# Optimization experiments

Hardware: AMD Instinct MI355X
Metric: run time of the kernel (lower is better)

Reference implementation:

```python
import jax, jax.numpy as jnp
import numpy as np
import math

B, N, C = 8, 4096, 768
H = 12
DH = C // H
M = 256
LN_EPS = 1e-5


def setup_inputs() -> dict:
    key = jax.random.key(0)
    ks = jax.random.split(key, 7)
    x = jax.random.normal(ks[0], (B, N, C), dtype=jnp.float32)
    # torch Linear weight [out,in]; store transposed for y = x @ W
    W_qkv = jax.random.normal(ks[1], (C, 3 * C), dtype=jnp.float32) * (1.0 / math.sqrt(C))
    W_proj = jax.random.normal(ks[2], (C, C), dtype=jnp.float32) * (1.0 / math.sqrt(C))
    b_proj = jnp.zeros((C,), dtype=jnp.float32)
    gamma = jnp.ones((C,), dtype=jnp.float32)
    beta = jnp.zeros((C,), dtype=jnp.float32)
    random_features = jax.random.normal(ks[3], (M, DH), dtype=jnp.float32) / math.sqrt(DH)
    return {"x": x, "W_qkv": W_qkv, "W_proj": W_proj, "b_proj": b_proj,
            "gamma": gamma, "beta": beta, "random_features": random_features}


def _phi(t, random_features):
    # t: [B, H, N, DH] -> [B, H, N, M]; phi(x) = exp(w·x - ||x||^2/2) / sqrt(M)
    norm_sq = 0.5 * jnp.sum(t * t, axis=-1, keepdims=True)
    proj = jnp.einsum('bhnd,md->bhnm', t, random_features)
    return jnp.exp(proj - norm_sq) * (1.0 / math.sqrt(M))


def reference(x, W_qkv, W_proj, b_proj, gamma, beta, random_features):
    b, n, c = x.shape
    qkv = (x @ W_qkv).reshape(b, n, 3, H, DH)
    qkv = jnp.transpose(qkv, (2, 0, 3, 1, 4))  # [3, B, H, N, DH]
    q, k, v = qkv[0], qkv[1], qkv[2]

    q_p = _phi(q, random_features)  # [B,H,N,M]
    k_p = _phi(k, random_features)  # [B,H,N,M]

    kv = jnp.einsum('bhnm,bhnd->bhmd', k_p, v)       # [B,H,M,DH]
    out = jnp.einsum('bhnm,bhmd->bhnd', q_p, kv)     # [B,H,N,DH]

    k_sum = jnp.sum(k_p, axis=2)                      # [B,H,M]
    normalizer = jnp.einsum('bhnm,bhm->bhn', q_p, k_sum)[..., None]
    out = out / (normalizer + 1e-6)

    x_attn = jnp.transpose(out, (0, 2, 1, 3)).reshape(b, n, c)
    x_attn = x_attn @ W_proj + b_proj
    # dropout is identity in eval / p=0

    y = x + x_attn
    mu = jnp.mean(y, axis=-1, keepdims=True)
    var = jnp.mean(jnp.square(y - mu), axis=-1, keepdims=True)
    return (y - mu) * jax.lax.rsqrt(var + LN_EPS) * gamma + beta
```

## Files before the change

kernel.cpp:

```cpp
#include <hip/hip_runtime.h>
#include <hip/hip_fp16.h>


#define LOG2E 1.44269504088896340736f

typedef _Float16 half8 __attribute__((ext_vector_type(8)));
typedef _Float16 half4_t __attribute__((ext_vector_type(4)));
typedef _Float16 half2_t __attribute__((ext_vector_type(2)));
typedef float f32x4 __attribute__((ext_vector_type(4)));

#if __has_builtin(__builtin_amdgcn_fdot2)
#define FDOT2(a, b, c) __builtin_amdgcn_fdot2((a), (b), (c), false)
#else
#define FDOT2(a, b, c) \
  ((float)(a)[0] * (float)(b)[0] + ((float)(a)[1] * (float)(b)[1] + (c)))
#endif

static __device__ __forceinline__ half2_t pk2(float a, float b) {
#if __has_builtin(__builtin_amdgcn_cvt_pkrtz)
  return __builtin_bit_cast(half2_t, __builtin_amdgcn_cvt_pkrtz(a, b));
#else
  half2_t r; r[0] = (_Float16)a; r[1] = (_Float16)b; return r;
#endif
}

__device__ __forceinline__ void glds16(const _Float16* g, _Float16* s) {
  __builtin_amdgcn_global_load_lds(
      (const __attribute__((address_space(1))) void*)g,
      (__attribute__((address_space(3))) unsigned int*)s,
      16, 0, 0);
}


__global__ __launch_bounds__(256)
void prep(const float* __restrict__ x, const float* __restrict__ Wqkv,
          const float* __restrict__ Wproj, const float* __restrict__ rfm,
          _Float16* __restrict__ x_h, _Float16* __restrict__ wqkvT,
          _Float16* __restrict__ wprojT, _Float16* __restrict__ rfh) {
  const long bid = blockIdx.x;
  if (bid < 24576) {
    long i = (bid * 256 + threadIdx.x) * 4;
    float4 v = *(const float4*)(x + i);
    half4_t h;
    h[0] = (_Float16)v.x; h[1] = (_Float16)v.y; h[2] = (_Float16)v.z; h[3] = (_Float16)v.w;
    *(half4_t*)(x_h + i) = h;
    return;
  }
  long idx = (bid - 24576) * 256 + threadIdx.x;
  if (idx < 1769472) {
    int k = (int)(idx / 2304), n = (int)(idx % 2304);
    wqkvT[(long)n * 768 + k] = (_Float16)Wqkv[idx];
  } else if ((idx -= 1769472) < 589824) {
    int k = (int)(idx / 768), n = (int)(idx % 768);
    wprojT[(long)n * 768 + k] = (_Float16)Wproj[idx];
  } else if ((idx -= 589824) < 16384) {
    rfh[idx] = (_Float16)rfm[idx];
  }
}


__global__ __launch_bounds__(256)
void gemm_qkv(const _Float16* __restrict__ W, const _Float16* __restrict__ X,
              _Float16* __restrict__ qh, _Float16* __restrict__ kh,
              _Float16* __restrict__ vT,
              float* __restrict__ nsqLq, float* __restrict__ nsqLk) {
  __shared__ __align__(16) _Float16 As[128 * 32];
  __shared__ __align__(16) _Float16 Bs[128 * 32];
  const int tid = threadIdx.x;
  const int w = tid >> 6, l = tid & 63;
  const int lr = l & 15, kg = l >> 4;
  const int m0 = blockIdx.x * 128;
  const int n0 = blockIdx.y * 128;
  const int wm = (w >> 1) * 64, wn = (w & 1) * 64;

  const _Float16* gA = W + (long)(m0 + w * 32 + (l >> 2)) * 768 + (l & 3) * 8;
  const _Float16* gB = X + (long)(n0 + w * 32 + (l >> 2)) * 768 + (l & 3) * 8;
  _Float16* sA = As + (w * 32) * 32;
  _Float16* sB = Bs + (w * 32) * 32;

  f32x4 acc[4][4];
#pragma unroll
  for (int t = 0; t < 4; ++t)
#pragma unroll
    for (int u = 0; u < 4; ++u) acc[t][u] = (f32x4){0.f, 0.f, 0.f, 0.f};

  for (int kc = 0; kc < 24; ++kc) {
    __syncthreads();
    glds16(gA, sA);
    glds16(gA + 16 * 768, sA + 16 * 32);
    glds16(gB, sB);
    glds16(gB + 16 * 768, sB + 16 * 32);
    gA += 32; gB += 32;
    __syncthreads();

    half8 af[4], bf[4];
#pragma unroll
    for (int t = 0; t < 4; ++t)
      af[t] = *(const half8*)(As + (wm + t * 16 + lr) * 32 + kg * 8);
#pragma unroll
    for (int u = 0; u < 4; ++u)
      bf[u] = *(const half8*)(Bs + (wn + u * 16 + lr) * 32 + kg * 8);
#pragma unroll
    for (int t = 0; t < 4; ++t)
#pragma unroll
      for (int u = 0; u < 4; ++u)
        acc[t][u] = __builtin_amdgcn_mfma_f32_16x16x32_f16(af[t], bf[u], acc[t][u], 0, 0, 0);
  }

  const int which = (m0 >= 1536) ? 2 : ((m0 >= 768) ? 1 : 0);
  const int base = (m0 - which * 768) + wm;
  const int h = base >> 6;

  if (which < 2) {
    _Float16* dst = (which == 0) ? qh : kh;
    float* nd = (which == 0) ? nsqLq : nsqLk;
    float ns[4] = {0.f, 0.f, 0.f, 0.f};
#pragma unroll
    for (int u = 0; u < 4; ++u) {
      const int tok = n0 + wn + u * 16 + lr;
      const int b_ = tok >> 12, n_ = tok & 4095;
      const long rowbase = ((long)(b_ * 12 + h) * 4096 + n_) * 64;
#pragma unroll
      for (int t = 0; t < 4; ++t) {
        half2_t h01 = pk2(acc[t][u][0], acc[t][u][1]);
        half2_t h23 = pk2(acc[t][u][2], acc[t][u][3]);
        half4_t p4; p4[0] = h01[0]; p4[1] = h01[1]; p4[2] = h23[0]; p4[3] = h23[1];
        *(half4_t*)(dst + rowbase + t * 16 + kg * 4) = p4;
#pragma unroll
        for (int r = 0; r < 4; ++r) { float f = (float)p4[r]; ns[u] += f * f; }
      }
    }
#pragma unroll
    for (int u = 0; u < 4; ++u) {
      float s = ns[u];
      s += __shfl_xor(s, 16);
      s += __shfl_xor(s, 32);
      if (kg == 0) {
        const int tok = n0 + wn + u * 16 + lr;
        const int b_ = tok >> 12, n_ = tok & 4095;
        nd[(long)(b_ * 12 + h) * 4096 + n_] = 0.5f * s * LOG2E + 4.0f;
      }
    }
  } else {
#pragma unroll
    for (int u = 0; u < 4; ++u) {
      const int tok = n0 + wn + u * 16 + lr;
      const int b_ = tok >> 12, n_ = tok & 4095;
      const long hb = (long)(b_ * 12 + h) * 64;
#pragma unroll
      for (int t = 0; t < 4; ++t)
#pragma unroll
        for (int r = 0; r < 4; ++r)
          vT[(hb + t * 16 + kg * 4 + r) * 4096 + n_] = (_Float16)acc[t][u][r];
    }
  }
}


__global__ __launch_bounds__(256)
void gemm_proj(const _Float16* __restrict__ A, const _Float16* __restrict__ BT,
               float* __restrict__ Co, const float* __restrict__ bias,
               const float* __restrict__ resid) {
  __shared__ __align__(16) _Float16 As[128 * 32];
  __shared__ __align__(16) _Float16 Bs[128 * 32];
  const int tid = threadIdx.x;
  const int w = tid >> 6, l = tid & 63;
  const int lr = l & 15, kg = l >> 4;
  const int m0 = blockIdx.y * 128;
  const int n0 = blockIdx.x * 128;
  const int wm = (w >> 1) * 64, wn = (w & 1) * 64;

  const _Float16* gA = A + (long)(m0 + w * 32 + (l >> 2)) * 768 + (l & 3) * 8;
  const _Float16* gB = BT + (long)(n0 + w * 32 + (l >> 2)) * 768 + (l & 3) * 8;
  _Float16* sA = As + (w * 32) * 32;
  _Float16* sB = Bs + (w * 32) * 32;

  f32x4 acc[4][4];
#pragma unroll
  for (int t = 0; t < 4; ++t)
#pragma unroll
    for (int u = 0; u < 4; ++u) acc[t][u] = (f32x4){0.f, 0.f, 0.f, 0.f};

  for (int kc = 0; kc < 24; ++kc) {
    __syncthreads();
    glds16(gA, sA);
    glds16(gA + 16 * 768, sA + 16 * 32);
    glds16(gB, sB);
    glds16(gB + 16 * 768, sB + 16 * 32);
    gA += 32; gB += 32;
    __syncthreads();

    half8 af[4], bf[4];
#pragma unroll
    for (int t = 0; t < 4; ++t)
      af[t] = *(const half8*)(As + (wm + t * 16 + lr) * 32 + kg * 8);
#pragma unroll
    for (int u = 0; u < 4; ++u)
      bf[u] = *(const half8*)(Bs + (wn + u * 16 + lr) * 32 + kg * 8);
#pragma unroll
    for (int t = 0; t < 4; ++t)
#pragma unroll
      for (int u = 0; u < 4; ++u)
        acc[t][u] = __builtin_amdgcn_mfma_f32_16x16x32_f16(af[t], bf[u], acc[t][u], 0, 0, 0);
  }

#pragma unroll
  for (int u = 0; u < 4; ++u) {
    const int col = n0 + wn + u * 16 + lr;
    const float bv = bias[col];
#pragma unroll
    for (int t = 0; t < 4; ++t) {
      const int row = m0 + wm + t * 16 + kg * 4;
#pragma unroll
      for (int r = 0; r < 4; ++r) {
        long idx = (long)(row + r) * 768 + col;
        Co[idx] = acc[t][u][r] + bv + resid[idx];
      }
    }
  }
}


__global__ __launch_bounds__(256)
void kv_fused(const _Float16* __restrict__ kh, const _Float16* __restrict__ vT,
              const _Float16* __restrict__ rfh, const float* __restrict__ nsqLk,
              _Float16* __restrict__ kvpart, float* __restrict__ kspart) {
  __shared__ __align__(16) _Float16 Ka[64 * 32], Kb[64 * 32];
  __shared__ __align__(16) _Float16 Va[64 * 32], Vb[64 * 32];
  __shared__ __align__(16) _Float16 P[256 * 72];
  const int chunk = blockIdx.x, bh = blockIdx.y;
  const int tid = threadIdx.x, w = tid >> 6, l = tid & 63;
  const int lr = l & 15, kg = l >> 4;
  const long khbase = (long)bh * 4096 * 64;
  const long vtbase = (long)bh * 64 * 4096;
  const half2_t ONES = {(_Float16)1.f, (_Float16)1.f};

  half8 rf[4][2];
#pragma unroll
  for (int u = 0; u < 4; ++u)
#pragma unroll
    for (int ks = 0; ks < 2; ++ks)
      rf[u][ks] = *(const half8*)(rfh + (w * 64 + u * 16 + lr) * 64 + ks * 32 + kg * 8);

  f32x4 kvacc[4][4];
#pragma unroll
  for (int mt = 0; mt < 4; ++mt)
#pragma unroll
    for (int dt = 0; dt < 4; ++dt) kvacc[mt][dt] = (f32x4){0.f, 0.f, 0.f, 0.f};
  float ksacc[4] = {0.f, 0.f, 0.f, 0.f};

  for (int t8 = 0; t8 < 8; ++t8) {
    const int nt = chunk * 512 + t8 * 64;
    __syncthreads();
    if (w == 0) {
#pragma unroll
      for (int j = 0; j < 4; ++j)
        glds16(kh + khbase + (long)(nt + j * 16 + (l >> 2)) * 64 + (l & 3) * 8, Ka + j * 512);
    } else if (w == 1) {
#pragma unroll
      for (int j = 0; j < 4; ++j)
        glds16(kh + khbase + (long)(nt + j * 16 + (l >> 2)) * 64 + 32 + (l & 3) * 8, Kb + j * 512);
    } else if (w == 2) {
#pragma unroll
      for (int j = 0; j < 4; ++j)
        glds16(vT + vtbase + (long)(j * 16 + (l >> 2)) * 4096 + nt + (l & 3) * 8, Va + j * 512);
    } else {
#pragma unroll
      for (int j = 0; j < 4; ++j)
        glds16(vT + vtbase + (long)(j * 16 + (l >> 2)) * 4096 + nt + 32 + (l & 3) * 8, Vb + j * 512);
    }
    __syncthreads();

    half8 af[4][2];
#pragma unroll
    for (int tt = 0; tt < 4; ++tt) {
      af[tt][0] = *(const half8*)(Ka + (tt * 16 + lr) * 32 + kg * 8);
      af[tt][1] = *(const half8*)(Kb + (tt * 16 + lr) * 32 + kg * 8);
    }
    f32x4 sacc[4][4];
#pragma unroll
    for (int tt = 0; tt < 4; ++tt)
#pragma unroll
      for (int u = 0; u < 4; ++u) sacc[tt][u] = (f32x4){0.f, 0.f, 0.f, 0.f};
#pragma unroll
    for (int ks = 0; ks < 2; ++ks)
#pragma unroll
      for (int tt = 0; tt < 4; ++tt)
#pragma unroll
        for (int u = 0; u < 4; ++u)
          sacc[tt][u] = __builtin_amdgcn_mfma_f32_16x16x32_f16(af[tt][ks], rf[u][ks],
                                                               sacc[tt][u], 0, 0, 0);
    float4 nsq4[4];
#pragma unroll
    for (int tt = 0; tt < 4; ++tt)
      nsq4[tt] = *(const float4*)(nsqLk + (long)bh * 4096 + nt + tt * 16 + kg * 4);
#pragma unroll
    for (int tt = 0; tt < 4; ++tt)
#pragma unroll
      for (int u = 0; u < 4; ++u) {
        float e0 = exp2f(sacc[tt][u][0] * LOG2E - nsq4[tt].x);
        float e1 = exp2f(sacc[tt][u][1] * LOG2E - nsq4[tt].y);
        float e2 = exp2f(sacc[tt][u][2] * LOG2E - nsq4[tt].z);
        float e3 = exp2f(sacc[tt][u][3] * LOG2E - nsq4[tt].w);
        half2_t h01 = pk2(e0, e1), h23 = pk2(e2, e3);
        half4_t p4; p4[0] = h01[0]; p4[1] = h01[1]; p4[2] = h23[0]; p4[3] = h23[1];
        *(half4_t*)(P + (w * 64 + u * 16 + lr) * 72 + tt * 16 + kg * 4) = p4;
      }
#pragma unroll
    for (int ks = 0; ks < 2; ++ks) {
      half8 pa[4], bv[4];
#pragma unroll
      for (int mt = 0; mt < 4; ++mt)
        pa[mt] = *(const half8*)(P + (w * 64 + mt * 16 + lr) * 72 + ks * 32 + kg * 8);
#pragma unroll
      for (int dt = 0; dt < 4; ++dt)
        bv[dt] = *(const half8*)((ks == 0 ? Va : Vb) + (dt * 16 + lr) * 32 + kg * 8);
#pragma unroll
      for (int mt = 0; mt < 4; ++mt)
#pragma unroll
        for (int dt = 0; dt < 4; ++dt)
          kvacc[mt][dt] = __builtin_amdgcn_mfma_f32_16x16x32_f16(pa[mt], bv[dt],
                                                                 kvacc[mt][dt], 0, 0, 0);
#pragma unroll
      for (int mt = 0; mt < 4; ++mt) {
        const half2_t* pp = (const half2_t*)&pa[mt];
#pragma unroll
        for (int p = 0; p < 4; ++p) ksacc[mt] = FDOT2(pp[p], ONES, ksacc[mt]);
      }
    }
  }

#pragma unroll
  for (int mt = 0; mt < 4; ++mt) {
    float v = ksacc[mt];
    v += __shfl_xor(v, 16);
    v += __shfl_xor(v, 32);
    if (l < 16) kspart[((bh * 8 + chunk) << 8) + w * 64 + mt * 16 + l] = v;
  }
#pragma unroll
  for (int mt = 0; mt < 4; ++mt)
#pragma unroll
    for (int dt = 0; dt < 4; ++dt)
#pragma unroll
      for (int r = 0; r < 4; ++r)
        kvpart[(((long)(bh * 8 + chunk) * 256) + w * 64 + mt * 16 + kg * 4 + r) * 64 +
               dt * 16 + lr] = (_Float16)kvacc[mt][dt][r];
}


__global__ __launch_bounds__(256)
void reduce_all(const _Float16* __restrict__ kvpart, const float* __restrict__ kspart,
                _Float16* __restrict__ kvT, _Float16* __restrict__ ksumh) {
  if (blockIdx.x < 6144) {
    long i = (long)blockIdx.x * 256 + threadIdx.x;
    const int bh = (int)(i >> 14);
    const int rem = (int)(i & 16383);
    const int m = rem >> 6, d = rem & 63;
    float s = 0.f;
#pragma unroll
    for (int c = 0; c < 8; ++c)
      s += (float)kvpart[(((long)bh * 8 + c) * 256 + m) * 64 + d];
    kvT[(long)bh * 16384 + d * 256 + m] = (_Float16)s;
  } else {
    int i = (blockIdx.x - 6144) * 256 + threadIdx.x;
    int bh = i >> 8, m = i & 255;
    float s = 0.f;
#pragma unroll
    for (int c = 0; c < 8; ++c) s += kspart[((bh * 8 + c) << 8) + m];
    ksumh[i] = (_Float16)s;
  }
}


__global__ __launch_bounds__(256)
void attn_fused(const _Float16* __restrict__ qh, const _Float16* __restrict__ rfh,
                const float* __restrict__ nsqLq, const _Float16* __restrict__ kvT,
                const _Float16* __restrict__ ksumh, _Float16* __restrict__ attn) {
  __shared__ __align__(16) _Float16 Qa[64 * 32], Qb[64 * 32];
  __shared__ __align__(16) _Float16 KV[64 * 264];
  __shared__ __align__(16) _Float16 KS[256];
  __shared__ __align__(16) _Float16 P[64 * 264];
  __shared__ __align__(16) float NS[64];
  const int chunk = blockIdx.x, bh = blockIdx.y;
  const int b = bh / 12, h = bh % 12;
  const int tid = threadIdx.x, w = tid >> 6, l = tid & 63;
  const int lr = l & 15, kg = l >> 4;

  {
    const int d = tid >> 2, mb = (tid & 3) * 64;
#pragma unroll
    for (int j = 0; j < 8; ++j)
      *(half8*)(KV + d * 264 + mb + j * 8) =
          *(const half8*)(kvT + (long)bh * 16384 + d * 256 + mb + j * 8);
    if (tid < 32) *(half8*)(KS + tid * 8) = *(const half8*)(ksumh + bh * 256 + tid * 8);
  }

  half8 rf[4][2];
#pragma unroll
  for (int mt = 0; mt < 4; ++mt)
#pragma unroll
    for (int ks = 0; ks < 2; ++ks)
      rf[mt][ks] = *(const half8*)(rfh + (w * 64 + mt * 16 + lr) * 64 + ks * 32 + kg * 8);

  for (int t8 = 0; t8 < 4; ++t8) {
    const int nt = chunk * 256 + t8 * 64;
    __syncthreads();
    if (w == 0) {
#pragma unroll
      for (int j = 0; j < 4; ++j)
        glds16(qh + ((long)bh * 4096 + nt + j * 16 + (l >> 2)) * 64 + (l & 3) * 8, Qa + j * 512);
    } else if (w == 1) {
#pragma unroll
      for (int j = 0; j < 4; ++j)
        glds16(qh + ((long)bh * 4096 + nt + j * 16 + (l >> 2)) * 64 + 32 + (l & 3) * 8, Qb + j * 512);
    }
    __syncthreads();

    half8 bq[4][2];
#pragma unroll
    for (int tt = 0; tt < 4; ++tt) {
      bq[tt][0] = *(const half8*)(Qa + (tt * 16 + lr) * 32 + kg * 8);
      bq[tt][1] = *(const half8*)(Qb + (tt * 16 + lr) * 32 + kg * 8);
    }
    f32x4 sacc[4][4];
#pragma unroll
    for (int mt = 0; mt < 4; ++mt)
#pragma unroll
      for (int tt = 0; tt < 4; ++tt) sacc[mt][tt] = (f32x4){0.f, 0.f, 0.f, 0.f};
#pragma unroll
    for (int ks = 0; ks < 2; ++ks)
#pragma unroll
      for (int mt = 0; mt < 4; ++mt)
#pragma unroll
        for (int tt = 0; tt < 4; ++tt)
          sacc[mt][tt] = __builtin_amdgcn_mfma_f32_16x16x32_f16(rf[mt][ks], bq[tt][ks],
                                                                sacc[mt][tt], 0, 0, 0);
    float nsqv[4];
#pragma unroll
    for (int tt = 0; tt < 4; ++tt)
      nsqv[tt] = nsqLq[(long)bh * 4096 + nt + tt * 16 + lr];
#pragma unroll
    for (int mt = 0; mt < 4; ++mt)
#pragma unroll
      for (int tt = 0; tt < 4; ++tt) {
        float e0 = exp2f(sacc[mt][tt][0] * LOG2E - nsqv[tt]);
        float e1 = exp2f(sacc[mt][tt][1] * LOG2E - nsqv[tt]);
        float e2 = exp2f(sacc[mt][tt][2] * LOG2E - nsqv[tt]);
        float e3 = exp2f(sacc[mt][tt][3] * LOG2E - nsqv[tt]);
        half2_t h01 = pk2(e0, e1), h23 = pk2(e2, e3);
        half4_t p4; p4[0] = h01[0]; p4[1] = h01[1]; p4[2] = h23[0]; p4[3] = h23[1];
        *(half4_t*)(P + (tt * 16 + lr) * 264 + w * 64 + mt * 16 + kg * 4) = p4;
      }
    __syncthreads();

    f32x4 oacc[4];
#pragma unroll
    for (int u = 0; u < 4; ++u) oacc[u] = (f32x4){0.f, 0.f, 0.f, 0.f};
    float nacc = 0.f;
#pragma unroll
    for (int ks = 0; ks < 8; ++ks) {
      half8 ap = *(const half8*)(P + (w * 16 + lr) * 264 + ks * 32 + kg * 8);
      half8 kv8 = *(const half8*)(KS + ks * 32 + kg * 8);
      const half2_t* a2 = (const half2_t*)&ap;
      const half2_t* k2 = (const half2_t*)&kv8;
#pragma unroll
      for (int p = 0; p < 4; ++p) nacc = FDOT2(a2[p], k2[p], nacc);
#pragma unroll
      for (int u = 0; u < 4; ++u) {
        half8 bkv = *(const half8*)(KV + (u * 16 + lr) * 264 + ks * 32 + kg * 8);
        oacc[u] = __builtin_amdgcn_mfma_f32_16x16x32_f16(ap, bkv, oacc[u], 0, 0, 0);
      }
    }
    nacc += __shfl_xor(nacc, 16);
    nacc += __shfl_xor(nacc, 32);
    if (l < 16) NS[w * 16 + l] = nacc;
    f32x4 n4 = *(const f32x4*)(NS + w * 16 + kg * 4);
    float inv[4];
#pragma unroll
    for (int r = 0; r < 4; ++r) inv[r] = 1.f / (n4[r] + 1e-6f);
#pragma unroll
    for (int u = 0; u < 4; ++u)
#pragma unroll
      for (int r = 0; r < 4; ++r)
        attn[((long)b * 4096 + nt + w * 16 + kg * 4 + r) * 768 + h * 64 + u * 16 + lr] =
            (_Float16)(oacc[u][r] * inv[r]);
  }
}


__global__ __launch_bounds__(256)
void ln_kernel(const float* __restrict__ y, const float* __restrict__ gamma,
               const float* __restrict__ beta, float* __restrict__ outp) {
  const int wv = threadIdx.x >> 6, l = threadIdx.x & 63;
  const long row = (long)blockIdx.x * 4 + wv;
  const float* yr = y + row * 768;
  float v[12];
  float s = 0.f;
#pragma unroll
  for (int j = 0; j < 12; ++j) { v[j] = yr[l + j * 64]; s += v[j]; }
#pragma unroll
  for (int off = 32; off; off >>= 1) s += __shfl_xor(s, off);
  const float mu = s * (1.f / 768.f);
  float vs = 0.f;
#pragma unroll
  for (int j = 0; j < 12; ++j) { float d = v[j] - mu; vs += d * d; }
#pragma unroll
  for (int off = 32; off; off >>= 1) vs += __shfl_xor(vs, off);
  const float rstd = rsqrtf(vs * (1.f / 768.f) + 1e-5f);
  float* orp = outp + row * 768;
#pragma unroll
  for (int j = 0; j < 12; ++j)
    orp[l + j * 64] = (v[j] - mu) * rstd * gamma[l + j * 64] + beta[l + j * 64];
}


extern "C" void kernel_launch(void* const* d_in, const int* in_sizes, int n_in,
                              void* d_out, int out_size, void* d_ws, size_t ws_size,
                              hipStream_t stream) {
  const float* x = (const float*)d_in[0];
  const float* Wqkv = (const float*)d_in[1];
  const float* Wproj = (const float*)d_in[2];
  const float* bproj = (const float*)d_in[3];
  const float* gamma = (const float*)d_in[4];
  const float* beta = (const float*)d_in[5];
  const float* rfm = (const float*)d_in[6];

  char* ws = (char*)d_ws;
  size_t off = 0;
  auto alloc = [&](size_t bytes) -> void* {
    void* p = ws + off;
    off += (bytes + 255) & ~(size_t)255;
    return p;
  };
  char* regionA = (char*)alloc(50331648ULL);
  _Float16* x_h = (_Float16*)regionA;
  _Float16* kvpart = (_Float16*)regionA;
  _Float16* attn = (_Float16*)regionA;

  _Float16* wqkvT = (_Float16*)alloc(1769472ULL * 2);
  _Float16* wprojT = (_Float16*)alloc(589824ULL * 2);
  _Float16* rfh = (_Float16*)alloc(16384ULL * 2);
  _Float16* qh = (_Float16*)alloc(25165824ULL * 2);
  _Float16* kh = (_Float16*)alloc(25165824ULL * 2);
  _Float16* vT = (_Float16*)alloc(25165824ULL * 2);
  float* nsqLq = (float*)alloc(393216ULL * 4);
  float* nsqLk = (float*)alloc(393216ULL * 4);
  float* kspart = (float*)alloc(96ULL * 8 * 256 * 4);
  _Float16* kvT = (_Float16*)alloc(96ULL * 16384 * 2);
  _Float16* ksumh = (_Float16*)alloc(96ULL * 256 * 2);

  float* y = (float*)d_out;

  prep<<<33856, 256, 0, stream>>>(x, Wqkv, Wproj, rfm, x_h, wqkvT, wprojT, rfh);
  gemm_qkv<<<dim3(18, 256), 256, 0, stream>>>(wqkvT, x_h, qh, kh, vT, nsqLq, nsqLk);
  kv_fused<<<dim3(8, 96), 256, 0, stream>>>(kh, vT, rfh, nsqLk, kvpart, kspart);
  reduce_all<<<6240, 256, 0, stream>>>(kvpart, kspart, kvT, ksumh);
  attn_fused<<<dim3(16, 96), 256, 0, stream>>>(qh, rfh, nsqLq, kvT, ksumh, attn);
  gemm_proj<<<dim3(6, 256), 256, 0, stream>>>(attn, wprojT, y, bproj, x);
  ln_kernel<<<8192, 256, 0, stream>>>(y, gamma, beta, y);
}
```

Before: 620.7 us.

## Rewrite QKV GEMM as 256x256 double-buffered pipelined tile with swizzled LDS

The QKV projection GEMM moves from a 128x128 tile with a 32-wide K step and two barriers per step to a 256x256 tile, 512 threads and a 64-wide K step. LDS is double-buffered, and half-tile async global-to-LDS loads are interleaved between four MFMA quadrant phases, using explicit vmcnt waits and setprio. LDS rows are XOR-swizzled to avoid bank conflicts, and block IDs are remapped so that neighbouring blocks share tiles across XCDs. The epilogue now reduces the per-head norms through LDS. The larger tile raises data reuse but uses 128KB of LDS and 128 accumulator registers per thread, which lowers occupancy.

After: 612.9 us. No clear change (-1.3%).

```diff
diff --git a/kernel.cpp b/kernel.cpp
--- a/kernel.cpp
+++ b/kernel.cpp
@@ -59,99 +59,208 @@
 }
 
 
-__global__ __launch_bounds__(256)
+__device__ __forceinline__ void stage_unit(const _Float16* __restrict__ G, int grow0,
+                                           int kcol, _Float16* lds, int w, int l) {
+#pragma unroll
+  for (int j = 0; j < 2; ++j) {
+    const int ci = w + j * 8;
+    const int row = ci * 8 + (l >> 3);
+    const int col8 = (l & 7) ^ (row & 7);
+    glds16(G + (long)(grow0 + row) * 768 + kcol + col8 * 8, lds + ci * 512);
+  }
+}
+
+static __device__ __forceinline__ half8 ldsw(const _Float16* buf, int r, int sl) {
+  return *(const half8*)(buf + r * 64 + ((sl ^ (r & 7)) << 3));
+}
+
+__global__ __launch_bounds__(512)
 void gemm_qkv(const _Float16* __restrict__ W, const _Float16* __restrict__ X,
               _Float16* __restrict__ qh, _Float16* __restrict__ kh,
               _Float16* __restrict__ vT,
               float* __restrict__ nsqLq, float* __restrict__ nsqLk) {
-  __shared__ __align__(16) _Float16 As[128 * 32];
-  __shared__ __align__(16) _Float16 Bs[128 * 32];
+  __shared__ __align__(16) _Float16 As[32768];
+  __shared__ __align__(16) _Float16 Bs[32768];
   const int tid = threadIdx.x;
   const int w = tid >> 6, l = tid & 63;
   const int lr = l & 15, kg = l >> 4;
-  const int m0 = blockIdx.x * 128;
-  const int n0 = blockIdx.y * 128;
-  const int wm = (w >> 1) * 64, wn = (w & 1) * 64;
-
-  const _Float16* gA = W + (long)(m0 + w * 32 + (l >> 2)) * 768 + (l & 3) * 8;
-  const _Float16* gB = X + (long)(n0 + w * 32 + (l >> 2)) * 768 + (l & 3) * 8;
-  _Float16* sA = As + (w * 32) * 32;
-  _Float16* sB = Bs + (w * 32) * 32;
-
-  f32x4 acc[4][4];
-#pragma unroll
-  for (int t = 0; t < 4; ++t)
+  const int wr = w >> 2, wc = w & 3;
+
+  const int bid = blockIdx.x;
+  const int wg = (bid & 7) * 144 + (bid >> 3);
+  const int m0 = (wg % 9) * 256;
+  const int n0 = (wg / 9) * 256;
+
+  stage_unit(W, m0,       0,  As,         w, l);
+  stage_unit(X, n0,       0,  Bs,         w, l);
+  stage_unit(X, n0 + 128, 0,  Bs + 8192,  w, l);
+  stage_unit(W, m0 + 128, 0,  As + 8192,  w, l);
+  stage_unit(W, m0,       64, As + 16384, w, l);
+  stage_unit(X, n0,       64, Bs + 16384, w, l);
+  stage_unit(X, n0 + 128, 64, Bs + 24576, w, l);
+  asm volatile("s_waitcnt vmcnt(6)" ::: "memory");
+  __builtin_amdgcn_s_barrier();
+
+  f32x4 acc[8][4];
+#pragma unroll
+  for (int t = 0; t < 8; ++t)
 #pragma unroll
     for (int u = 0; u < 4; ++u) acc[t][u] = (f32x4){0.f, 0.f, 0.f, 0.f};
 
-  for (int kc = 0; kc < 24; ++kc) {
-    __syncthreads();
-    glds16(gA, sA);
-    glds16(gA + 16 * 768, sA + 16 * 32);
-    glds16(gB, sB);
-    glds16(gB + 16 * 768, sB + 16 * 32);
-    gA += 32; gB += 32;
-    __syncthreads();
-
-    half8 af[4], bf[4];
-#pragma unroll
-    for (int t = 0; t < 4; ++t)
-      af[t] = *(const half8*)(As + (wm + t * 16 + lr) * 32 + kg * 8);
-#pragma unroll
-    for (int u = 0; u < 4; ++u)
-      bf[u] = *(const half8*)(Bs + (wn + u * 16 + lr) * 32 + kg * 8);
-#pragma unroll
-    for (int t = 0; t < 4; ++t)
-#pragma unroll
-      for (int u = 0; u < 4; ++u)
-        acc[t][u] = __builtin_amdgcn_mfma_f32_16x16x32_f16(af[t], bf[u], acc[t][u], 0, 0, 0);
+  for (int kt = 0; kt < 12; ++kt) {
+    const int c = kt & 1, o = c ^ 1;
+    const _Float16* Ac = As + c * 16384;
+    const _Float16* Bc = Bs + c * 16384;
+    half8 aR[4][2], bR0[2][2], bR1[2][2];
+
+#pragma unroll
+    for (int i = 0; i < 4; ++i) {
+      const int r = wr * 16 + i * 32 + lr;
+      aR[i][0] = ldsw(Ac, r, kg);
+      aR[i][1] = ldsw(Ac, r, 4 + kg);
+    }
+#pragma unroll
+    for (int j = 0; j < 2; ++j) {
+      const int r = wc * 16 + j * 64 + lr;
+      bR0[j][0] = ldsw(Bc, r, kg);
+      bR0[j][1] = ldsw(Bc, r, 4 + kg);
+    }
+    if (kt + 1 < 12)
+      stage_unit(W, m0 + 128, (kt + 1) * 64, As + o * 16384 + 8192, w, l);
+    __builtin_amdgcn_s_barrier();
+    __builtin_amdgcn_s_setprio(1);
+#pragma unroll
+    for (int ks = 0; ks < 2; ++ks)
+#pragma unroll
+      for (int i = 0; i < 4; ++i)
+#pragma unroll
+        for (int j = 0; j < 2; ++j)
+          acc[i][j] = __builtin_amdgcn_mfma_f32_16x16x32_f16(aR[i][ks], bR0[j][ks],
+                                                             acc[i][j], 0, 0, 0);
+    __builtin_amdgcn_s_setprio(0);
+    __builtin_amdgcn_s_barrier();
+
+#pragma unroll
+    for (int j = 0; j < 2; ++j) {
+      const int r = 128 + wc * 16 + j * 64 + lr;
+      bR1[j][0] = ldsw(Bc, r, kg);
+      bR1[j][1] = ldsw(Bc, r, 4 + kg);
+    }
+    if (kt + 2 < 12)
+      stage_unit(W, m0, (kt + 2) * 64, As + c * 16384, w, l);
+    __builtin_amdgcn_s_barrier();
+    __builtin_amdgcn_s_setprio(1);
+#pragma unroll
+    for (int ks = 0; ks < 2; ++ks)
+#pragma unroll
+      for (int i = 0; i < 4; ++i)
+#pragma unroll
+        for (int j = 0; j < 2; ++j)
+          acc[i][2 + j] = __builtin_amdgcn_mfma_f32_16x16x32_f16(aR[i][ks], bR1[j][ks],
+                                                                 acc[i][2 + j], 0, 0, 0);
+    __builtin_amdgcn_s_setprio(0);
+    __builtin_amdgcn_s_barrier();
+
+#pragma unroll
+    for (int i = 0; i < 4; ++i) {
+      const int r = 128 + wr * 16 + i * 32 + lr;
+      aR[i][0] = ldsw(Ac, r, kg);
+      aR[i][1] = ldsw(Ac, r, 4 + kg);
+    }
+    if (kt + 2 < 12)
+      stage_unit(X, n0, (kt + 2) * 64, Bs + c * 16384, w, l);
+    __builtin_amdgcn_s_barrier();
+    __builtin_amdgcn_s_setprio(1);
+#pragma unroll
+    for (int ks = 0; ks < 2; ++ks)
+#pragma unroll
+      for (int i = 0; i < 4; ++i)
+#pragma unroll
+        for (int j = 0; j < 2; ++j)
+          acc[4 + i][2 + j] = __builtin_amdgcn_mfma_f32_16x16x32_f16(aR[i][ks], bR1[j][ks],
+                                                                     acc[4 + i][2 + j], 0, 0, 0);
+    __builtin_amdgcn_s_setprio(0);
+    __builtin_amdgcn_s_barrier();
+
+    if (kt + 2 < 12)
+      stage_unit(X, n0 + 128, (kt + 2) * 64, Bs + c * 16384 + 8192, w, l);
+    if (kt < 10)
+      asm volatile("s_waitcnt vmcnt(6)" ::: "memory");
+    else
+      asm volatile("s_waitcnt vmcnt(0)" ::: "memory");
+    __builtin_amdgcn_s_barrier();
+    __builtin_amdgcn_s_setprio(1);
+#pragma unroll
+    for (int ks = 0; ks < 2; ++ks)
+#pragma unroll
+      for (int i = 0; i < 4; ++i)
+#pragma unroll
+        for (int j = 0; j < 2; ++j)
+          acc[4 + i][j] = __builtin_amdgcn_mfma_f32_16x16x32_f16(aR[i][ks], bR0[j][ks],
+                                                                 acc[4 + i][j], 0, 0, 0);
+    __builtin_amdgcn_s_setprio(0);
+    __builtin_amdgcn_s_barrier();
   }
 
   const int which = (m0 >= 1536) ? 2 : ((m0 >= 768) ? 1 : 0);
-  const int base = (m0 - which * 768) + wm;
-  const int h = base >> 6;
+  const int hbase = (m0 - which * 768) >> 6;
+  const int b_ = n0 >> 12;
+  const int nb = n0 & 4095;
 
   if (which < 2) {
-    _Float16* dst = (which == 0) ? qh : kh;
-    float* nd = (which == 0) ? nsqLq : nsqLk;
-    float ns[4] = {0.f, 0.f, 0.f, 0.f};
-#pragma unroll
-    for (int u = 0; u < 4; ++u) {
-      const int tok = n0 + wn + u * 16 + lr;
-      const int b_ = tok >> 12, n_ = tok & 4095;
-      const long rowbase = ((long)(b_ * 12 + h) * 4096 + n_) * 64;
-#pragma unroll
-      for (int t = 0; t < 4; ++t) {
+    _Float16* dst = which ? kh : qh;
+    float* nd = which ? nsqLk : nsqLq;
+    float ns[4][4];
+#pragma unroll
+    for (int a = 0; a < 4; ++a)
+#pragma unroll
+      for (int b2 = 0; b2 < 4; ++b2) ns[a][b2] = 0.f;
+#pragma unroll
+    for (int t = 0; t < 8; ++t) {
+      const int h = hbase + (t >> 1);
+      const int d0 = wr * 16 + (t & 1) * 32 + kg * 4;
+#pragma unroll
+      for (int u = 0; u < 4; ++u) {
+        const int n_ = nb + wc * 16 + u * 64 + lr;
         half2_t h01 = pk2(acc[t][u][0], acc[t][u][1]);
         half2_t h23 = pk2(acc[t][u][2], acc[t][u][3]);
         half4_t p4; p4[0] = h01[0]; p4[1] = h01[1]; p4[2] = h23[0]; p4[3] = h23[1];
-        *(half4_t*)(dst + rowbase + t * 16 + kg * 4) = p4;
-#pragma unroll
-        for (int r = 0; r < 4; ++r) { float f = (float)p4[r]; ns[u] += f * f; }
-      }
-    }
-#pragma unroll
-    for (int u = 0; u < 4; ++u) {
-      float s = ns[u];
-      s += __shfl_xor(s, 16);
-      s += __shfl_xor(s, 32);
-      if (kg == 0) {
-        const int tok = n0 + wn + u * 16 + lr;
-        const int b_ = tok >> 12, n_ = tok & 4095;
-        nd[(long)(b_ * 12 + h) * 4096 + n_] = 0.5f * s * LOG2E + 4.0f;
-      }
+        *(half4_t*)(dst + ((long)(b_ * 12 + h) * 4096 + n_) * 64 + d0) = p4;
+#pragma unroll
+        for (int r = 0; r < 4; ++r) { float f = (float)p4[r]; ns[t >> 1][u] += f * f; }
+      }
+    }
+    float* nsP = (float*)As;
+#pragma unroll
+    for (int h2 = 0; h2 < 4; ++h2)
+#pragma unroll
+      for (int u = 0; u < 4; ++u) {
+        float s = ns[h2][u];
+        s += __shfl_xor(s, 16);
+        s += __shfl_xor(s, 32);
+        if (kg == 0) nsP[wr * 1024 + h2 * 256 + wc * 16 + u * 64 + lr] = s;
+      }
+    __syncthreads();
+#pragma unroll
+    for (int e = 0; e < 2; ++e) {
+      const int idx = tid + e * 512;
+      const int h2 = idx >> 8, tk = idx & 255;
+      const float vsum = nsP[h2 * 256 + tk] + nsP[1024 + h2 * 256 + tk];
+      nd[(long)(b_ * 12 + hbase + h2) * 4096 + nb + tk] = 0.5f * vsum * LOG2E + 4.0f;
     }
   } else {
 #pragma unroll
-    for (int u = 0; u < 4; ++u) {
-      const int tok = n0 + wn + u * 16 + lr;
-      const int b_ = tok >> 12, n_ = tok & 4095;
+    for (int t = 0; t < 8; ++t) {
+      const int h = hbase + (t >> 1);
       const long hb = (long)(b_ * 12 + h) * 64;
-#pragma unroll
-      for (int t = 0; t < 4; ++t)
+      const int d0 = wr * 16 + (t & 1) * 32 + kg * 4;
+#pragma unroll
+      for (int u = 0; u < 4; ++u) {
+        const int n_ = nb + wc * 16 + u * 64 + lr;
 #pragma unroll
         for (int r = 0; r < 4; ++r)
-          vT[(hb + t * 16 + kg * 4 + r) * 4096 + n_] = (_Float16)acc[t][u][r];
+          vT[(hb + d0 + r) * 4096 + n_] = (_Float16)acc[t][u][r];
+      }
     }
   }
 }
@@ -552,7 +661,7 @@
   float* y = (float*)d_out;
 
   prep<<<33856, 256, 0, stream>>>(x, Wqkv, Wproj, rfm, x_h, wqkvT, wprojT, rfh);
-  gemm_qkv<<<dim3(18, 256), 256, 0, stream>>>(wqkvT, x_h, qh, kh, vT, nsqLq, nsqLk);
+  gemm_qkv<<<1152, 512, 0, stream>>>(wqkvT, x_h, qh, kh, vT, nsqLq, nsqLk);
   kv_fused<<<dim3(8, 96), 256, 0, stream>>>(kh, vT, rfh, nsqLk, kvpart, kspart);
   reduce_all<<<6240, 256, 0, stream>>>(kvpart, kspart, kvT, ksumh);
   attn_fused<<<dim3(16, 96), 256, 0, stream>>>(qh, rfh, nsqLq, kvT, ksumh, attn);
```
